# Kernel tuning notes

Measured on AMD Instinct MI355X. Metric: run time of the kernel, lower is better.

The kernel has to match this reference:

```python
import jax, jax.numpy as jnp
import numpy as np

B, S, D, H = 2, 2048, 768, 12
HD = D // H  # head_dim = 64


def setup_inputs() -> dict:
    key = jax.random.key(0)
    ks = jax.random.split(key, 9)
    s = 1.0 / np.sqrt(D)
    return {
        "x": jax.random.normal(ks[0], (B, S, D), dtype=jnp.float32),
        "Wq": jax.random.normal(ks[1], (D, D), dtype=jnp.float32) * s,
        "bq": jnp.zeros((D,), dtype=jnp.float32),
        "Wk": jax.random.normal(ks[2], (D, D), dtype=jnp.float32) * s,
        "bk": jnp.zeros((D,), dtype=jnp.float32),
        "Wv": jax.random.normal(ks[3], (D, D), dtype=jnp.float32) * s,
        "bv": jnp.zeros((D,), dtype=jnp.float32),
        "Wo": jax.random.normal(ks[4], (D, D), dtype=jnp.float32) * s,
        "bo": jnpp if False else jnp.zeros((D,), dtype=jnp.float32),
    }


def reference(x, Wq, bq, Wk, bk, Wv, bv, Wo, bo):
    b, s, d = x.shape
    # projections, split heads: [b, h, s, hd]
    def proj(W, bias):
        y = x @ W + bias
        return y.reshape(b, s, H, HD).transpose(0, 2, 1, 3)

    q = proj(Wq, bq)
    k = proj(Wk, bk)
    v = proj(Wv, bv)

    scale = 1.0 / jnp.sqrt(jnp.float32(HD))
    scores = jnp.einsum("bhqd,bhkd->bhqk", q, k) * scale
    causal = jnp.tril(jnp.ones((s, s), dtype=bool))  # True where allowed
    scores = jnp.where(causal, scores, -jnp.inf)
    attn = jax.nn.softmax(scores, axis=-1)
    ctx = jnp.einsum("bhqk,bhkd->bhqd", attn, v)
    ctx = ctx.transpose(0, 2, 1, 3).reshape(b, s, d)
    return ctx @ Wo + bo
```

## Files before the change

### kernel.cpp

```cpp
#include <hip/hip_runtime.h>
#include <stdint.h>

typedef unsigned short u16;
typedef __attribute__((ext_vector_type(8))) short s16x8;
typedef __attribute__((ext_vector_type(4))) float f32x4;
typedef __attribute__((ext_vector_type(16))) float f32x16;

#define MFMA_BF16(a, b, c) __builtin_amdgcn_mfma_f32_16x16x32_bf16((a), (b), (c), 0, 0, 0)
#define MFMA32(a, b, c) __builtin_amdgcn_mfma_f32_32x32x16_bf16((a), (b), (c), 0, 0, 0)

typedef const __attribute__((address_space(1))) uint32_t* gas1_t;
typedef __attribute__((address_space(3))) uint32_t* las3_t;
#define GLDS16(dst, src) __builtin_amdgcn_global_load_lds((gas1_t)(src), (las3_t)(dst), 16, 0, 0)

static __device__ __forceinline__ u16 f2bf(float f) {
    uint32_t u = __float_as_uint(f);
    u = (u + 0x7fffu + ((u >> 16) & 1u)) >> 16;
    return (u16)u;
}
static __device__ __forceinline__ uint32_t pk2bf(float a, float b) {
    return (uint32_t)f2bf(a) | ((uint32_t)f2bf(b) << 16);
}
static __device__ __forceinline__ float bf2f(u16 h) {
    return __uint_as_float(((uint32_t)h) << 16);
}

__global__ void k_cvt_bf16(const float* __restrict__ in, u16* __restrict__ out) {
    int i = (blockIdx.x * 256 + threadIdx.x) * 8;
    f32x4 a = *(const f32x4*)(in + i);
    f32x4 b = *(const f32x4*)(in + i + 4);
    s16x8 r;
    r[0] = (short)f2bf(a[0]); r[1] = (short)f2bf(a[1]);
    r[2] = (short)f2bf(a[2]); r[3] = (short)f2bf(a[3]);
    r[4] = (short)f2bf(b[0]); r[5] = (short)f2bf(b[1]);
    r[6] = (short)f2bf(b[2]); r[7] = (short)f2bf(b[3]);
    *(s16x8*)(out + i) = r;
}

__global__ void k_transpose_w(const float* __restrict__ w0, const float* __restrict__ w1,
                              const float* __restrict__ w2, const float* __restrict__ w3,
                              u16* __restrict__ t0, u16* __restrict__ t1,
                              u16* __restrict__ t2, u16* __restrict__ t3) {
    __shared__ float tile[32][33];
    const float* W; u16* T;
    switch (blockIdx.z) {
        case 0:  W = w0; T = t0; break;
        case 1:  W = w1; T = t1; break;
        case 2:  W = w2; T = t2; break;
        default: W = w3; T = t3; break;
    }
    int n0 = blockIdx.x * 32, k0 = blockIdx.y * 32;
    int tx = threadIdx.x, ty = threadIdx.y;
#pragma unroll
    for (int i = 0; i < 4; ++i)
        tile[ty + 8 * i][tx] = W[(size_t)(k0 + ty + 8 * i) * 768 + n0 + tx];
    __syncthreads();
#pragma unroll
    for (int i = 0; i < 4; ++i)
        T[(size_t)(n0 + ty + 8 * i) * 768 + k0 + tx] = f2bf(tile[tx][ty + 8 * i]);
}

__global__ __launch_bounds__(256) void k_gemm_qkv(
        const u16* __restrict__ A,
        const u16* __restrict__ btq, const u16* __restrict__ btk, const u16* __restrict__ btv,
        const float* __restrict__ bq, const float* __restrict__ bk, const float* __restrict__ bv,
        u16* __restrict__ outq, u16* __restrict__ outk, u16* __restrict__ outv) {
    __shared__ u16 lA[128 * 64];
    __shared__ u16 lB[64 * 64];
    const int bx = blockIdx.x, sel = bx / 12, nb = bx - sel * 12;
    const u16* Bt; const float* bias;
    if (sel == 0)      { Bt = btq; bias = bq; }
    else if (sel == 1) { Bt = btk; bias = bk; }
    else               { Bt = btv; bias = bv; }
    const int t = threadIdx.x, lane = t & 63, w = t >> 6;
    const int wr = w >> 1, wc = w & 1;
    const int c = lane & 15, g = lane >> 4;
    const int m0 = blockIdx.y * 128, n0 = nb * 64;
    f32x4 acc[4][2] = {};
    const int lr = lane >> 3, lg = lane & 7;
    const int swz8 = 8 * (lg ^ lr);
    const u16* gA = A  + (size_t)(m0 + w * 8 + lr) * 768 + swz8;
    const u16* gB = Bt + (size_t)(n0 + w * 8 + lr) * 768 + swz8;
    for (int kb = 0; kb < 768; kb += 64) {
#pragma unroll
        for (int j = 0; j < 4; ++j)
            GLDS16(&lA[j * 2048 + w * 512], gA + (size_t)j * 32 * 768 + kb);
#pragma unroll
        for (int j = 0; j < 2; ++j)
            GLDS16(&lB[j * 2048 + w * 512], gB + (size_t)j * 32 * 768 + kb);
        __syncthreads();
#pragma unroll
        for (int kh = 0; kh < 2; ++kh) {
            s16x8 af[4], bfr[2];
            const int gg = kh * 4 + g;
#pragma unroll
            for (int i = 0; i < 4; ++i) {
                const int ra = wr * 64 + i * 16 + c;
                af[i] = *(const s16x8*)&lA[ra * 64 + 8 * (gg ^ (ra & 7))];
            }
#pragma unroll
            for (int j = 0; j < 2; ++j) {
                const int rb = wc * 32 + j * 16 + c;
                bfr[j] = *(const s16x8*)&lB[rb * 64 + 8 * (gg ^ (rb & 7))];
            }
#pragma unroll
            for (int i = 0; i < 4; ++i)
#pragma unroll
                for (int j = 0; j < 2; ++j)
                    acc[i][j] = MFMA_BF16(af[i], bfr[j], acc[i][j]);
        }
        __syncthreads();
    }
    const float C2 = 0.18033688011112042f;
    const int h = nb;
    if (sel < 2) {
        u16* outp = (sel == 0) ? outq : outk;
        const float osc = (sel == 0) ? C2 : 1.0f;
#pragma unroll
        for (int i = 0; i < 4; ++i)
#pragma unroll
            for (int j = 0; j < 2; ++j) {
                const int hd = wc * 32 + j * 16 + c;
                const float bvv = bias[n0 + hd];
#pragma unroll
                for (int rr = 0; rr < 4; ++rr) {
                    const int m = m0 + wr * 64 + i * 16 + g * 4 + rr;
                    const int b = m >> 11, s = m & 2047;
                    outp[(((size_t)(b * 12 + h) * 2048 + s) << 6) + hd] =
                        f2bf((acc[i][j][rr] + bvv) * osc);
                }
            }
    } else {
#pragma unroll
        for (int i = 0; i < 4; ++i)
#pragma unroll
            for (int j = 0; j < 2; ++j) {
                const int hd = wc * 32 + j * 16 + c;
                const float bvv = bias[n0 + hd];
                const int m = m0 + wr * 64 + i * 16 + g * 4;
                const int b = m >> 11, s = m & 2047;
                uint64_t pk = (uint64_t)pk2bf(acc[i][j][0] + bvv, acc[i][j][1] + bvv) |
                              ((uint64_t)pk2bf(acc[i][j][2] + bvv, acc[i][j][3] + bvv) << 32);
                *(uint64_t*)&outv[((size_t)(b * 12 + h) * 64 + hd) * 2048 + s] = pk;
            }
    }
}

__global__ __launch_bounds__(256) void k_gemm_out(const u16* __restrict__ A,
                                                  const u16* __restrict__ Bt,
                                                  const float* __restrict__ bias,
                                                  float* __restrict__ out) {
    __shared__ u16 lA[64 * 64];
    __shared__ u16 lB[64 * 64];
    const int t = threadIdx.x;
    const int lane = t & 63, w = t >> 6;
    const int wr = w >> 1, wc = w & 1;
    const int c = lane & 15, g = lane >> 4;
    const int m0 = blockIdx.y * 64, n0 = blockIdx.x * 64;
    f32x4 acc[2][2] = {};
    const int lr = lane >> 3, lq = lane & 7;
    const int sq = (lq ^ lr) * 8;
    const u16* gA0 = A  + (size_t)(m0 + w * 16 + lr) * 768 + sq;
    const u16* gA1 = gA0 + 8 * 768;
    const u16* gB0 = Bt + (size_t)(n0 + w * 16 + lr) * 768 + sq;
    const u16* gB1 = gB0 + 8 * 768;
    u16* dA0 = &lA[w * 1024];
    u16* dA1 = &lA[w * 1024 + 512];
    u16* dB0 = &lB[w * 1024];
    u16* dB1 = &lB[w * 1024 + 512];
    for (int kb = 0; kb < 768; kb += 64) {
        GLDS16(dA0, gA0 + kb); GLDS16(dA1, gA1 + kb);
        GLDS16(dB0, gB0 + kb); GLDS16(dB1, gB1 + kb);
        __syncthreads();
#pragma unroll
        for (int st = 0; st < 2; ++st) {
            s16x8 af[2], bf[2];
            const int col = st * 32 + g * 8;
#pragma unroll
            for (int i = 0; i < 2; ++i) {
                int ra = wr * 32 + i * 16 + c;
                af[i] = *(const s16x8*)&lA[ra * 64 + (col ^ ((ra & 7) << 3))];
                int rb = wc * 32 + i * 16 + c;
                bf[i] = *(const s16x8*)&lB[rb * 64 + (col ^ ((rb & 7) << 3))];
            }
#pragma unroll
            for (int i = 0; i < 2; ++i)
#pragma unroll
                for (int j = 0; j < 2; ++j)
                    acc[i][j] = MFMA_BF16(af[i], bf[j], acc[i][j]);
        }
        __syncthreads();
    }
#pragma unroll
    for (int i = 0; i < 2; ++i)
#pragma unroll
        for (int j = 0; j < 2; ++j) {
            const int n = n0 + wc * 32 + j * 16 + c;
            const float bvv = bias[n];
#pragma unroll
            for (int rr = 0; rr < 4; ++rr) {
                const int m = m0 + wr * 32 + i * 16 + g * 4 + rr;
                out[(size_t)m * 768 + n] = acc[i][j][rr] + bvv;
            }
        }
}

__global__ __launch_bounds__(128) void k_attn(const u16* __restrict__ qw,
                                              const u16* __restrict__ kw,
                                              const u16* __restrict__ vt,
                                              u16* __restrict__ ctxb,
                                              u16* __restrict__ pctx,
                                              float* __restrict__ pm,
                                              float* __restrict__ ps) {
    __shared__ u16 lK[2][64 * 64];
    __shared__ u16 lV[2][64 * 64];
    const int bid = blockIdx.x;
    const int slot = bid / 24, bh = bid - slot * 24;
    int qt64, seg;
    if (slot < 32)      { qt64 = 31 - (slot >> 2); seg = slot & 3; }
    else if (slot < 56) { const int u = slot - 32; const int d3 = u / 3; qt64 = 23 - d3; seg = u - d3 * 3; }
    else if (slot < 72) { const int u = slot - 56; qt64 = 15 - (u >> 1); seg = u & 1; }
    else                { qt64 = 79 - slot; seg = 0; }
    const int nseg = (qt64 >> 3) + 1;
    const int ch0 = seg * 8;
    const int nchunks = qt64 + 1 - ch0;
    const int nch = nchunks < 8 ? nchunks : 8;
    const int t = threadIdx.x, lane = t & 63, w = t >> 6;
    const int l31 = lane & 31, hi = lane >> 5;
    const int q0w = qt64 * 64 + w * 32;
    const u16* qp = qw + (size_t)bh * 2048 * 64;
    const u16* kp = kw + (size_t)bh * 2048 * 64;
    const u16* vp = vt + (size_t)bh * 64 * 2048;
    s16x8 qf[4];
#pragma unroll
    for (int dk = 0; dk < 4; ++dk)
        qf[dk] = *(const s16x8*)&qp[(size_t)(q0w + l31) * 64 + dk * 16 + hi * 8];
    asm volatile("s_waitcnt vmcnt(0)" ::: "memory");
    const int lr = lane >> 3, lg = lane & 7;
    const int swz8 = 8 * (lg ^ lr);
    const u16* kpb = kp + (size_t)(w * 8 + lr) * 64 + swz8;
    const u16* vpb = vp + (size_t)(w * 8 + lr) * 2048 + swz8;
    const int lastq = q0w + 31;
    f32x16 ct[2] = {};
    float m2 = -1e30f, ssum = 0.0f;
#define STAGE(bf, ch)                                                          \
    {                                                                          \
        const u16* ks_ = kpb + (size_t)(ch) * 4096;                            \
        GLDS16(&lK[bf][(w * 8) * 64], ks_);                                    \
        GLDS16(&lK[bf][(16 + w * 8) * 64], ks_ + 16 * 64);                     \
        GLDS16(&lK[bf][(32 + w * 8) * 64], ks_ + 32 * 64);                     \
        GLDS16(&lK[bf][(48 + w * 8) * 64], ks_ + 48 * 64);                     \
        const u16* vs_ = vpb + (size_t)(ch) * 64;                              \
        GLDS16(&lV[bf][(w * 8) * 64], vs_);                                    \
        GLDS16(&lV[bf][(16 + w * 8) * 64], vs_ + 16 * 2048);                   \
        GLDS16(&lV[bf][(32 + w * 8) * 64], vs_ + 32 * 2048);                   \
        GLDS16(&lV[bf][(48 + w * 8) * 64], vs_ + 48 * 2048);                   \
    }
    STAGE(0, ch0);
    for (int ci = 0; ci < nch; ++ci) {
        const int bf = ci & 1, Kc = (ch0 + ci) * 64;
        if (ci + 1 < nch) {
            STAGE(bf ^ 1, ch0 + ci + 1);
            asm volatile("s_waitcnt vmcnt(8)" ::: "memory");
        } else {
            asm volatile("s_waitcnt vmcnt(0)" ::: "memory");
        }
        __builtin_amdgcn_sched_barrier(0);
        __builtin_amdgcn_s_barrier();
        if (Kc <= lastq) {
            f32x16 st[2] = {};
            __builtin_amdgcn_s_setprio(1);
#pragma unroll
            for (int dk = 0; dk < 4; ++dk) {
                const int gr = dk * 2 + hi;
                const int r0 = l31, r1 = 32 + l31;
                s16x8 kf0 = *(const s16x8*)&lK[bf][r0 * 64 + 8 * (gr ^ (r0 & 7))];
                s16x8 kf1 = *(const s16x8*)&lK[bf][r1 * 64 + 8 * (gr ^ (r1 & 7))];
                st[0] = MFMA32(kf0, qf[dk], st[0]);
                st[1] = MFMA32(kf1, qf[dk], st[1]);
            }
            __builtin_amdgcn_s_setprio(0);
            const int qg = q0w + l31;
            float tv[32];
            if (Kc + 63 <= q0w) {
#pragma unroll
                for (int j = 0; j < 16; ++j) { tv[j] = st[0][j]; tv[16 + j] = st[1][j]; }
            } else {
                const int kb = Kc + 4 * hi;
#pragma unroll
                for (int j = 0; j < 16; ++j) {
                    const int kloc = (j & 3) + 8 * (j >> 2);
                    tv[j]      = (kb + kloc      <= qg) ? st[0][j] : -1e30f;
                    tv[16 + j] = (kb + kloc + 32 <= qg) ? st[1][j] : -1e30f;
                }
            }
            float x16[16], x8[8], x4[4];
#pragma unroll
            for (int j = 0; j < 16; ++j) x16[j] = fmaxf(tv[j], tv[j + 16]);
#pragma unroll
            for (int j = 0; j < 8; ++j) x8[j] = fmaxf(x16[j], x16[j + 8]);
#pragma unroll
            for (int j = 0; j < 4; ++j) x4[j] = fmaxf(x8[j], x8[j + 4]);
            const float mt = fmaxf(fmaxf(x4[0], x4[1]), fmaxf(x4[2], x4[3]));
            if (!__all(mt <= m2 + 8.0f)) {
                float mq = fmaxf(mt, __shfl_xor(mt, 32));
                const float mnew = fmaxf(m2, mq);
                const float fac = __builtin_amdgcn_exp2f(m2 - mnew);
                ssum *= fac;
#pragma unroll
                for (int j = 0; j < 16; ++j) { ct[0][j] *= fac; ct[1][j] *= fac; }
                m2 = mnew;
            }
            float p[32];
#pragma unroll
            for (int j = 0; j < 32; ++j) p[j] = __builtin_amdgcn_exp2f(tv[j] - m2);
            float y16[16], y8[8], y4[4];
#pragma unroll
            for (int j = 0; j < 16; ++j) y16[j] = p[j] + p[j + 16];
#pragma unroll
            for (int j = 0; j < 8; ++j) y8[j] = y16[j] + y16[j + 8];
#pragma unroll
            for (int j = 0; j < 4; ++j) y4[j] = y8[j] + y8[j + 4];
            ssum += (y4[0] + y4[1]) + (y4[2] + y4[3]);
#pragma unroll
            for (int kt = 0; kt < 2; ++kt) {
                uint32_t pcv[8];
#pragma unroll
                for (int x = 0; x < 8; ++x) {
                    const int j = kt * 16 + 4 * (x >> 1) + 2 * (x & 1);
                    asm volatile("v_cvt_pk_bf16_f32 %0, %1, %2"
                                 : "=v"(pcv[x]) : "v"(p[j]), "v"(p[j + 1]));
                }
#pragma unroll
                for (int kl = 0; kl < 2; ++kl) {
                    uint32_t a0 = pcv[4 * kl],     b0 = pcv[4 * kl + 2];
                    uint32_t a1 = pcv[4 * kl + 1], b1 = pcv[4 * kl + 3];
                    asm volatile("v_permlane32_swap_b32 %0, %1" : "+v"(a0), "+v"(b0));
                    asm volatile("v_permlane32_swap_b32 %0, %1" : "+v"(a1), "+v"(b1));
                    union { uint32_t u[4]; s16x8 v; } pf;
                    pf.u[0] = a0; pf.u[1] = a1; pf.u[2] = b0; pf.u[3] = b1;
                    const int gr = (kt * 2 + kl) * 2 + hi;
                    const int rv0 = l31, rv1 = 32 + l31;
                    s16x8 vf0 = *(const s16x8*)&lV[bf][rv0 * 64 + 8 * (gr ^ (rv0 & 7))];
                    s16x8 vf1 = *(const s16x8*)&lV[bf][rv1 * 64 + 8 * (gr ^ (rv1 & 7))];
                    __builtin_amdgcn_s_setprio(1);
                    ct[0] = MFMA32(vf0, pf.v, ct[0]);
                    ct[1] = MFMA32(vf1, pf.v, ct[1]);
                    __builtin_amdgcn_s_setprio(0);
                }
            }
        }
        __builtin_amdgcn_s_barrier();
    }
    if (nseg == 1) {
        ssum += __shfl_xor(ssum, 32);
        const float inv = 1.0f / ssum;
        const int b = bh / 12, h = bh - b * 12;
        const size_t base = (size_t)(b * 2048 + q0w + l31) * 768 + h * 64;
#pragma unroll
        for (int ht = 0; ht < 2; ++ht)
#pragma unroll
            for (int a = 0; a < 4; ++a) {
                const int hd = ht * 32 + 8 * a + 4 * hi;
                uint64_t pk = (uint64_t)pk2bf(ct[ht][4 * a] * inv, ct[ht][4 * a + 1] * inv) |
                              ((uint64_t)pk2bf(ct[ht][4 * a + 2] * inv, ct[ht][4 * a + 3] * inv) << 32);
                *(uint64_t*)&ctxb[base + hd] = pk;
            }
    } else {
        const float srow = ssum + __shfl_xor(ssum, 32);
        const int ti = (bh * 32 + qt64) * 4 + seg;
        const int row = w * 32 + l31;
        u16* pp = &pctx[(size_t)ti * 4096 + row * 64];
#pragma unroll
        for (int ht = 0; ht < 2; ++ht)
#pragma unroll
            for (int a = 0; a < 4; ++a) {
                const int hd = ht * 32 + 8 * a + 4 * hi;
                uint64_t pk = (uint64_t)pk2bf(ct[ht][4 * a], ct[ht][4 * a + 1]) |
                              ((uint64_t)pk2bf(ct[ht][4 * a + 2], ct[ht][4 * a + 3]) << 32);
                *(uint64_t*)&pp[hd] = pk;
            }
        if (hi == 0) {
            pm[ti * 64 + row] = m2;
            ps[ti * 64 + row] = srow;
        }
    }
#undef STAGE
}

__global__ __launch_bounds__(256) void k_attn_combine(const u16* __restrict__ pctx,
                                                      const float* __restrict__ pm,
                                                      const float* __restrict__ ps,
                                                      u16* __restrict__ ctxb) {
    const int bh = blockIdx.x, qt64 = blockIdx.y + 8;
    const int nseg = (qt64 >> 3) + 1;
    const int t = threadIdx.x, row = t >> 2, h0 = (t & 3) * 16;
    const int tb = (bh * 32 + qt64) * 4;
    float mv[4], sv[4];
#pragma unroll
    for (int s = 0; s < 4; ++s) {
        mv[s] = (s < nseg) ? pm[(tb + s) * 64 + row] : -1e30f;
        sv[s] = (s < nseg) ? ps[(tb + s) * 64 + row] : 0.0f;
    }
    const float mstar = fmaxf(fmaxf(mv[0], mv[1]), fmaxf(mv[2], mv[3]));
    float wv[4], S = 0.0f;
#pragma unroll
    for (int s = 0; s < 4; ++s) {
        wv[s] = __builtin_amdgcn_exp2f(mv[s] - mstar);
        S += wv[s] * sv[s];
    }
    float acc[16] = {};
#pragma unroll
    for (int s = 0; s < 4; ++s) {
        if (s < nseg) {
            const u16* pp = &pctx[(size_t)(tb + s) * 4096 + row * 64 + h0];
            const float wgt = wv[s];
#pragma unroll
            for (int e = 0; e < 2; ++e) {
                s16x8 v = *(const s16x8*)(pp + e * 8);
#pragma unroll
                for (int x = 0; x < 8; ++x)
                    acc[e * 8 + x] += wgt * bf2f((u16)v[x]);
            }
        }
    }
    const float inv = 1.0f / S;
    const int b = bh / 12, h = bh - b * 12;
    u16* op = &ctxb[(size_t)(b * 2048 + qt64 * 64 + row) * 768 + h * 64 + h0];
    s16x8 o0, o1;
#pragma unroll
    for (int x = 0; x < 8; ++x) {
        o0[x] = (short)f2bf(acc[x] * inv);
        o1[x] = (short)f2bf(acc[8 + x] * inv);
    }
    *(s16x8*)op = o0;
    *(s16x8*)(op + 8) = o1;
}

extern "C" void kernel_launch(void* const* d_in, const int* in_sizes, int n_in,
                              void* d_out, int out_size, void* d_ws, size_t ws_size,
                              hipStream_t stream) {
    (void)in_sizes; (void)n_in; (void)out_size; (void)ws_size;
    const float* x  = (const float*)d_in[0];
    const float* Wq = (const float*)d_in[1];
    const float* bq = (const float*)d_in[2];
    const float* Wk = (const float*)d_in[3];
    const float* bk = (const float*)d_in[4];
    const float* Wv = (const float*)d_in[5];
    const float* bv = (const float*)d_in[6];
    const float* Wo = (const float*)d_in[7];
    const float* bo = (const float*)d_in[8];
    char* ws = (char*)d_ws;
    u16* xb   = (u16*)(ws);
    u16* wqt  = (u16*)(ws + 6291456);
    u16* wkt  = (u16*)(ws + 7471104);
    u16* wvt  = (u16*)(ws + 8650752);
    u16* wot  = (u16*)(ws + 9830400);
    u16* qwv  = (u16*)(ws + 11010048);
    u16* kwv  = (u16*)(ws + 17301504);
    u16* vtw  = (u16*)(ws + 23592960);
    u16* ctx  = (u16*)(ws + 29884416);
    u16* pctx = (u16*)(ws + 36175872);
    float* pm = (float*)(ws + 61341696);
    float* psu= (float*)(ws + 62128128);
    float* out = (float*)d_out;

    k_cvt_bf16<<<1536, 256, 0, stream>>>(x, xb);
    k_transpose_w<<<dim3(24, 24, 4), dim3(32, 8), 0, stream>>>(Wq, Wk, Wv, Wo, wqt, wkt, wvt, wot);
    k_gemm_qkv<<<dim3(36, 32), 256, 0, stream>>>(xb, wqt, wkt, wvt, bq, bk, bv, qwv, kwv, vtw);
    k_attn<<<1920, 128, 0, stream>>>(qwv, kwv, vtw, ctx, pctx, pm, psu);
    k_attn_combine<<<dim3(24, 24), 256, 0, stream>>>(pctx, pm, psu, ctx);
    k_gemm_out<<<dim3(12, 64), 256, 0, stream>>>(ctx, wot, bo, out);
}
```

Baseline: 162.1 us.

## Fuse prep kernels, swizzle GEMM grids for XCDs, enlarge attention query tiles

Merges the x-to-bf16 conversion and weight transpose into one launch, removing one kernel launch. Remaps the flat block ids of both GEMMs with a stride-8 swizzle so neighbouring tiles land on the same XCD and share L2. The attention kernel moves from 64-row to 128-row query tiles with 4 waves per block, using a table-driven causal split-K schedule. The combine kernel is resized to match. Larger attention tiles halve K/V reloads per query row, at the cost of fewer blocks and coarser load balance.

```diff
diff --git a/kernel.cpp b/kernel.cpp
--- a/kernel.cpp
+++ b/kernel.cpp
@@ -25,32 +25,36 @@
     return __uint_as_float(((uint32_t)h) << 16);
 }
 
-__global__ void k_cvt_bf16(const float* __restrict__ in, u16* __restrict__ out) {
-    int i = (blockIdx.x * 256 + threadIdx.x) * 8;
-    f32x4 a = *(const f32x4*)(in + i);
-    f32x4 b = *(const f32x4*)(in + i + 4);
-    s16x8 r;
-    r[0] = (short)f2bf(a[0]); r[1] = (short)f2bf(a[1]);
-    r[2] = (short)f2bf(a[2]); r[3] = (short)f2bf(a[3]);
-    r[4] = (short)f2bf(b[0]); r[5] = (short)f2bf(b[1]);
-    r[6] = (short)f2bf(b[2]); r[7] = (short)f2bf(b[3]);
-    *(s16x8*)(out + i) = r;
-}
-
-__global__ void k_transpose_w(const float* __restrict__ w0, const float* __restrict__ w1,
-                              const float* __restrict__ w2, const float* __restrict__ w3,
-                              u16* __restrict__ t0, u16* __restrict__ t1,
-                              u16* __restrict__ t2, u16* __restrict__ t3) {
+__global__ __launch_bounds__(256) void k_prep(const float* __restrict__ x, u16* __restrict__ xb,
+                                              const float* __restrict__ w0, const float* __restrict__ w1,
+                                              const float* __restrict__ w2, const float* __restrict__ w3,
+                                              u16* __restrict__ t0, u16* __restrict__ t1,
+                                              u16* __restrict__ t2, u16* __restrict__ t3) {
     __shared__ float tile[32][33];
+    const int bid = blockIdx.x, t = threadIdx.x;
+    if (bid < 1536) {
+        const int i = (bid * 256 + t) * 8;
+        f32x4 a = *(const f32x4*)(x + i);
+        f32x4 b = *(const f32x4*)(x + i + 4);
+        s16x8 r;
+        r[0] = (short)f2bf(a[0]); r[1] = (short)f2bf(a[1]);
+        r[2] = (short)f2bf(a[2]); r[3] = (short)f2bf(a[3]);
+        r[4] = (short)f2bf(b[0]); r[5] = (short)f2bf(b[1]);
+        r[6] = (short)f2bf(b[2]); r[7] = (short)f2bf(b[3]);
+        *(s16x8*)(xb + i) = r;
+        return;
+    }
+    const int u = bid - 1536;
+    const int z = u / 576, r2 = u - z * 576;
     const float* W; u16* T;
-    switch (blockIdx.z) {
+    switch (z) {
         case 0:  W = w0; T = t0; break;
         case 1:  W = w1; T = t1; break;
         case 2:  W = w2; T = t2; break;
         default: W = w3; T = t3; break;
     }
-    int n0 = blockIdx.x * 32, k0 = blockIdx.y * 32;
-    int tx = threadIdx.x, ty = threadIdx.y;
+    const int n0 = (r2 % 24) * 32, k0 = (r2 / 24) * 32;
+    const int tx = t & 31, ty = t >> 5;
 #pragma unroll
     for (int i = 0; i < 4; ++i)
         tile[ty + 8 * i][tx] = W[(size_t)(k0 + ty + 8 * i) * 768 + n0 + tx];
@@ -67,7 +71,10 @@
         u16* __restrict__ outq, u16* __restrict__ outk, u16* __restrict__ outv) {
     __shared__ u16 lA[128 * 64];
     __shared__ u16 lB[64 * 64];
-    const int bx = blockIdx.x, sel = bx / 12, nb = bx - sel * 12;
+    const int cid = blockIdx.x;
+    const int swz = (cid & 7) * 144 + (cid >> 3);
+    const int sx = swz % 36, by = swz / 36;
+    const int sel = sx / 12, nb = sx - sel * 12;
     const u16* Bt; const float* bias;
     if (sel == 0)      { Bt = btq; bias = bq; }
     else if (sel == 1) { Bt = btk; bias = bk; }
@@ -75,7 +82,7 @@
     const int t = threadIdx.x, lane = t & 63, w = t >> 6;
     const int wr = w >> 1, wc = w & 1;
     const int c = lane & 15, g = lane >> 4;
-    const int m0 = blockIdx.y * 128, n0 = nb * 64;
+    const int m0 = by * 128, n0 = nb * 64;
     f32x4 acc[4][2] = {};
     const int lr = lane >> 3, lg = lane & 7;
     const int swz8 = 8 * (lg ^ lr);
@@ -152,11 +159,14 @@
                                                   float* __restrict__ out) {
     __shared__ u16 lA[64 * 64];
     __shared__ u16 lB[64 * 64];
+    const int cid = blockIdx.x;
+    const int swz = (cid & 7) * 96 + (cid >> 3);
+    const int bx = swz % 12, by = swz / 12;
     const int t = threadIdx.x;
     const int lane = t & 63, w = t >> 6;
     const int wr = w >> 1, wc = w & 1;
     const int c = lane & 15, g = lane >> 4;
-    const int m0 = blockIdx.y * 64, n0 = blockIdx.x * 64;
+    const int m0 = by * 64, n0 = bx * 64;
     f32x4 acc[2][2] = {};
     const int lr = lane >> 3, lq = lane & 7;
     const int sq = (lq ^ lr) * 8;
@@ -205,7 +215,14 @@
         }
 }
 
-__global__ __launch_bounds__(128) void k_attn(const u16* __restrict__ qw,
+__device__ static const signed char SLOT_QT[40] = {
+    15,15,15,15, 14,14,14,14, 13,13,13,13, 12,12,12,12,
+    11,11,11, 10,10,10, 9,9,9, 8,8,8, 7,7, 6,6, 5,5, 4,4, 3, 2, 1, 0};
+__device__ static const signed char SLOT_SEG[40] = {
+    0,1,2,3, 0,1,2,3, 0,1,2,3, 0,1,2,3,
+    0,1,2, 0,1,2, 0,1,2, 0,1,2, 0,1, 0,1, 0,1, 0,1, 0, 0, 0, 0};
+
+__global__ __launch_bounds__(256) void k_attn(const u16* __restrict__ qw,
                                               const u16* __restrict__ kw,
                                               const u16* __restrict__ vt,
                                               u16* __restrict__ ctxb,
@@ -215,19 +232,16 @@
     __shared__ u16 lK[2][64 * 64];
     __shared__ u16 lV[2][64 * 64];
     const int bid = blockIdx.x;
-    const int slot = bid / 24, bh = bid - slot * 24;
-    int qt64, seg;
-    if (slot < 32)      { qt64 = 31 - (slot >> 2); seg = slot & 3; }
-    else if (slot < 56) { const int u = slot - 32; const int d3 = u / 3; qt64 = 23 - d3; seg = u - d3 * 3; }
-    else if (slot < 72) { const int u = slot - 56; qt64 = 15 - (u >> 1); seg = u & 1; }
-    else                { qt64 = 79 - slot; seg = 0; }
-    const int nseg = (qt64 >> 3) + 1;
+    const int slot = bid / 24, j24 = bid - slot * 24;
+    const int bh = (j24 & 7) * 3 + (j24 >> 3);
+    const int qt = SLOT_QT[slot], seg = SLOT_SEG[slot];
+    const int nseg = (2 * (qt + 1) + 7) >> 3;
     const int ch0 = seg * 8;
-    const int nchunks = qt64 + 1 - ch0;
-    const int nch = nchunks < 8 ? nchunks : 8;
+    const int rem = 2 * (qt + 1) - ch0;
+    const int nch = rem < 8 ? rem : 8;
     const int t = threadIdx.x, lane = t & 63, w = t >> 6;
     const int l31 = lane & 31, hi = lane >> 5;
-    const int q0w = qt64 * 64 + w * 32;
+    const int q0w = qt * 128 + w * 32;
     const u16* qp = qw + (size_t)bh * 2048 * 64;
     const u16* kp = kw + (size_t)bh * 2048 * 64;
     const u16* vp = vt + (size_t)bh * 64 * 2048;
@@ -238,30 +252,26 @@
     asm volatile("s_waitcnt vmcnt(0)" ::: "memory");
     const int lr = lane >> 3, lg = lane & 7;
     const int swz8 = 8 * (lg ^ lr);
-    const u16* kpb = kp + (size_t)(w * 8 + lr) * 64 + swz8;
-    const u16* vpb = vp + (size_t)(w * 8 + lr) * 2048 + swz8;
+    const u16* kpb = kp + (size_t)(w * 16 + lr) * 64 + swz8;
+    const u16* vpb = vp + (size_t)(w * 16 + lr) * 2048 + swz8;
     const int lastq = q0w + 31;
     f32x16 ct[2] = {};
     float m2 = -1e30f, ssum = 0.0f;
 #define STAGE(bf, ch)                                                          \
     {                                                                          \
         const u16* ks_ = kpb + (size_t)(ch) * 4096;                            \
-        GLDS16(&lK[bf][(w * 8) * 64], ks_);                                    \
-        GLDS16(&lK[bf][(16 + w * 8) * 64], ks_ + 16 * 64);                     \
-        GLDS16(&lK[bf][(32 + w * 8) * 64], ks_ + 32 * 64);                     \
-        GLDS16(&lK[bf][(48 + w * 8) * 64], ks_ + 48 * 64);                     \
+        GLDS16(&lK[bf][(w * 16) * 64], ks_);                                   \
+        GLDS16(&lK[bf][(w * 16 + 8) * 64], ks_ + 8 * 64);                      \
         const u16* vs_ = vpb + (size_t)(ch) * 64;                              \
-        GLDS16(&lV[bf][(w * 8) * 64], vs_);                                    \
-        GLDS16(&lV[bf][(16 + w * 8) * 64], vs_ + 16 * 2048);                   \
-        GLDS16(&lV[bf][(32 + w * 8) * 64], vs_ + 32 * 2048);                   \
-        GLDS16(&lV[bf][(48 + w * 8) * 64], vs_ + 48 * 2048);                   \
+        GLDS16(&lV[bf][(w * 16) * 64], vs_);                                   \
+        GLDS16(&lV[bf][(w * 16 + 8) * 64], vs_ + 8 * 2048);                    \
     }
     STAGE(0, ch0);
     for (int ci = 0; ci < nch; ++ci) {
         const int bf = ci & 1, Kc = (ch0 + ci) * 64;
         if (ci + 1 < nch) {
             STAGE(bf ^ 1, ch0 + ci + 1);
-            asm volatile("s_waitcnt vmcnt(8)" ::: "memory");
+            asm volatile("s_waitcnt vmcnt(4)" ::: "memory");
         } else {
             asm volatile("s_waitcnt vmcnt(0)" ::: "memory");
         }
@@ -368,9 +378,9 @@
             }
     } else {
         const float srow = ssum + __shfl_xor(ssum, 32);
-        const int ti = (bh * 32 + qt64) * 4 + seg;
+        const int ti = (bh * 16 + qt) * 4 + seg;
         const int row = w * 32 + l31;
-        u16* pp = &pctx[(size_t)ti * 4096 + row * 64];
+        u16* pp = &pctx[(size_t)ti * 8192 + row * 64];
 #pragma unroll
         for (int ht = 0; ht < 2; ++ht)
 #pragma unroll
@@ -381,8 +391,8 @@
                 *(uint64_t*)&pp[hd] = pk;
             }
         if (hi == 0) {
-            pm[ti * 64 + row] = m2;
-            ps[ti * 64 + row] = srow;
+            pm[ti * 128 + row] = m2;
+            ps[ti * 128 + row] = srow;
         }
     }
 #undef STAGE
@@ -392,49 +402,53 @@
                                                       const float* __restrict__ pm,
                                                       const float* __restrict__ ps,
                                                       u16* __restrict__ ctxb) {
-    const int bh = blockIdx.x, qt64 = blockIdx.y + 8;
-    const int nseg = (qt64 >> 3) + 1;
-    const int t = threadIdx.x, row = t >> 2, h0 = (t & 3) * 16;
-    const int tb = (bh * 32 + qt64) * 4;
-    float mv[4], sv[4];
-#pragma unroll
-    for (int s = 0; s < 4; ++s) {
-        mv[s] = (s < nseg) ? pm[(tb + s) * 64 + row] : -1e30f;
-        sv[s] = (s < nseg) ? ps[(tb + s) * 64 + row] : 0.0f;
-    }
-    const float mstar = fmaxf(fmaxf(mv[0], mv[1]), fmaxf(mv[2], mv[3]));
-    float wv[4], S = 0.0f;
-#pragma unroll
-    for (int s = 0; s < 4; ++s) {
-        wv[s] = __builtin_amdgcn_exp2f(mv[s] - mstar);
-        S += wv[s] * sv[s];
-    }
-    float acc[16] = {};
-#pragma unroll
-    for (int s = 0; s < 4; ++s) {
-        if (s < nseg) {
-            const u16* pp = &pctx[(size_t)(tb + s) * 4096 + row * 64 + h0];
-            const float wgt = wv[s];
-#pragma unroll
-            for (int e = 0; e < 2; ++e) {
-                s16x8 v = *(const s16x8*)(pp + e * 8);
-#pragma unroll
-                for (int x = 0; x < 8; ++x)
-                    acc[e * 8 + x] += wgt * bf2f((u16)v[x]);
-            }
-        }
-    }
-    const float inv = 1.0f / S;
+    const int bh = blockIdx.x, qt = blockIdx.y + 4;
+    const int nseg = (2 * (qt + 1) + 7) >> 3;
+    const int tb = (bh * 16 + qt) * 4;
     const int b = bh / 12, h = bh - b * 12;
-    u16* op = &ctxb[(size_t)(b * 2048 + qt64 * 64 + row) * 768 + h * 64 + h0];
-    s16x8 o0, o1;
-#pragma unroll
-    for (int x = 0; x < 8; ++x) {
-        o0[x] = (short)f2bf(acc[x] * inv);
-        o1[x] = (short)f2bf(acc[8 + x] * inv);
-    }
-    *(s16x8*)op = o0;
-    *(s16x8*)(op + 8) = o1;
+#pragma unroll
+    for (int it = 0; it < 2; ++it) {
+        const int u = threadIdx.x + it * 256;
+        const int row = u >> 2, h0 = (u & 3) * 16;
+        float mv[4], sv[4];
+#pragma unroll
+        for (int s = 0; s < 4; ++s) {
+            mv[s] = (s < nseg) ? pm[(tb + s) * 128 + row] : -1e30f;
+            sv[s] = (s < nseg) ? ps[(tb + s) * 128 + row] : 0.0f;
+        }
+        const float mstar = fmaxf(fmaxf(mv[0], mv[1]), fmaxf(mv[2], mv[3]));
+        float wv[4], S = 0.0f;
+#pragma unroll
+        for (int s = 0; s < 4; ++s) {
+            wv[s] = __builtin_amdgcn_exp2f(mv[s] - mstar);
+            S += wv[s] * sv[s];
+        }
+        float acc[16] = {};
+#pragma unroll
+        for (int s = 0; s < 4; ++s) {
+            if (s < nseg) {
+                const u16* pp = &pctx[(size_t)(tb + s) * 8192 + row * 64 + h0];
+                const float wgt = wv[s];
+#pragma unroll
+                for (int e = 0; e < 2; ++e) {
+                    s16x8 v = *(const s16x8*)(pp + e * 8);
+#pragma unroll
+                    for (int x = 0; x < 8; ++x)
+                        acc[e * 8 + x] += wgt * bf2f((u16)v[x]);
+                }
+            }
+        }
+        const float inv = 1.0f / S;
+        u16* op = &ctxb[(size_t)(b * 2048 + qt * 128 + row) * 768 + h * 64 + h0];
+        s16x8 o0, o1;
+#pragma unroll
+        for (int x = 0; x < 8; ++x) {
+            o0[x] = (short)f2bf(acc[x] * inv);
+            o1[x] = (short)f2bf(acc[8 + x] * inv);
+        }
+        *(s16x8*)op = o0;
+        *(s16x8*)(op + 8) = o1;
+    }
 }
 
 extern "C" void kernel_launch(void* const* d_in, const int* in_sizes, int n_in,
@@ -465,10 +479,9 @@
     float* psu= (float*)(ws + 62128128);
     float* out = (float*)d_out;
 
-    k_cvt_bf16<<<1536, 256, 0, stream>>>(x, xb);
-    k_transpose_w<<<dim3(24, 24, 4), dim3(32, 8), 0, stream>>>(Wq, Wk, Wv, Wo, wqt, wkt, wvt, wot);
-    k_gemm_qkv<<<dim3(36, 32), 256, 0, stream>>>(xb, wqt, wkt, wvt, bq, bk, bv, qwv, kwv, vtw);
-    k_attn<<<1920, 128, 0, stream>>>(qwv, kwv, vtw, ctx, pctx, pm, psu);
-    k_attn_combine<<<dim3(24, 24), 256, 0, stream>>>(pctx, pm, psu, ctx);
-    k_gemm_out<<<dim3(12, 64), 256, 0, stream>>>(ctx, wot, bo, out);
-}
+    k_prep<<<3840, 256, 0, stream>>>(x, xb, Wq, Wk, Wv, Wo, wqt, wkt, wvt, wot);
+    k_gemm_qkv<<<1152, 256, 0, stream>>>(xb, wqt, wkt, wvt, bq, bk, bv, qwv, kwv, vtw);
+    k_attn<<<960, 256, 0, stream>>>(qwv, kwv, vtw, ctx, pctx, pm, psu);
+    k_attn_combine<<<dim3(24, 12), 256, 0, stream>>>(pctx, pm, psu, ctx);
+    k_gemm_out<<<768, 256, 0, stream>>>(ctx, wot, bo, out);
+}
```

After: 160.6 us. Within noise of the previous version (-0.9%).
